# Kernel tuning notes

Measured on AMD Instinct MI355X. Metric: run time of the kernel, lower is better.

The kernel has to match this reference:

```python
import jax, jax.numpy as jnp
import numpy as np

N, D, H = 50000, 256, 8
C = D // H  # 32
E = 1600000
NEG_SLOPE = 0.2  # GATConv default leaky_relu slope
EPS = 1e-5


def setup_inputs() -> dict:
    key = jax.random.key(0)
    ks = jax.random.split(key, 8)
    x = jax.random.normal(ks[0], (N, D), dtype=jnp.float32)
    edge_index = jax.random.randint(ks[1], (2, E), 0, N, dtype=jnp.int32)
    # GATConv params: lin (no bias), att_src/att_dst, output bias
    scale = 1.0 / np.sqrt(D)
    W = jax.random.normal(ks[2], (D, H * C), dtype=jnp.float32) * scale
    att_src = jax.random.normal(ks[3], (H, C), dtype=jnp.float32) * scale
    att_dst = jax.random.normal(ks[4], (H, C), dtype=jnp.float32) * scale
    bias = jnp.zeros((H * C,), dtype=jnp.float32)
    ln_w = jnp.ones((D,), dtype=jnp.float32)
    ln_b = jnp.zeros((D,), dtype=jnp.float32)
    return {"x": x, "edge_index": edge_index, "W": W, "att_src": att_src,
            "att_dst": att_dst, "bias": bias, "ln_w": ln_w, "ln_b": ln_b}


def _gat_block(x, src, dst, W, att_src, att_dst, bias, ln_w, ln_b):
    n = x.shape[0]
    h = (x @ W).reshape(n, H, C)                      # [N,H,C]
    a_src = jnp.einsum('nhc,hc->nh', h, att_src)      # [N,H]
    a_dst = jnp.einsum('nhc,hc->nh', h, att_dst)      # [N,H]
    e = a_src[src] + a_dst[dst]                       # [E',H]
    e = jnp.where(e > 0, e, NEG_SLOPE * e)            # leaky_relu
    # segment softmax over incoming edges of each dst node
    m = jax.ops.segment_max(e, dst, num_segments=n)   # [N,H]
    m = jnp.where(jnp.isfinite(m), m, 0.0)
    ex = jnp.exp(e - m[dst])
    denom = jax.ops.segment_sum(ex, dst, num_segments=n)  # [N,H]
    alpha = ex / denom[dst]                           # [E',H] (self-loops => denom>0)
    msg = h[src] * alpha[..., None]                   # [E',H,C]
    out = jax.ops.segment_sum(msg, dst, num_segments=n).reshape(n, H * C) + bias
    # residual + LayerNorm
    y = out + x
    mu = y.mean(axis=-1, keepdims=True)
    var = y.var(axis=-1, keepdims=True)
    return (y - mu) / jnp.sqrt(var + EPS) * ln_w + ln_b


def reference(x, edge_index, W, att_src, att_dst, bias, ln_w, ln_b):
    n = x.shape[0]
    loop = jnp.arange(n, dtype=edge_index.dtype)      # GATConv adds self-loops by default
    src = jnp.concatenate([edge_index[0], loop])
    dst = jnp.concatenate([edge_index[1], loop])
    return _gat_block(x, src, dst, W, att_src, att_dst, bias, ln_w, ln_b)
```

## Files before the change

kernel.cpp:

```cpp
#include <hip/hip_runtime.h>

#define D_ 256
#define H_ 8
#define C_ 32
#define CAP_ 128
#define NEG_SLOPE 0.2f
#define EPS_ 1e-5f

typedef __attribute__((ext_vector_type(8))) short bf16x8;
typedef __attribute__((ext_vector_type(4))) float f32x4;
typedef __attribute__((ext_vector_type(2))) float f32x2;

__device__ __forceinline__ unsigned pk2(float a, float b) {
  unsigned ua = __float_as_uint(a), ub = __float_as_uint(b);
  ua = (ua + 0x7fffu + ((ua >> 16) & 1u)) >> 16;
  ub = (ub + 0x7fffu + ((ub >> 16) & 1u)) >> 16;
  return ua | (ub << 16);
}
__device__ __forceinline__ unsigned short f2b(float a) {
  unsigned ua = __float_as_uint(a);
  return (unsigned short)((ua + 0x7fffu + ((ua >> 16) & 1u)) >> 16);
}

#if defined(__has_builtin)
#if __has_builtin(__builtin_amdgcn_cvt_pk_fp8_f32) && __has_builtin(__builtin_amdgcn_cvt_pk_f32_fp8)
#define HW_FP8 1
#endif
#endif

__device__ __forceinline__ unsigned enc2_fp8(float a, float b) {
#ifdef HW_FP8
  return ((unsigned)__builtin_amdgcn_cvt_pk_fp8_f32(a, b, 0, false)) & 0xffffu;
#else
  unsigned r = 0;
  float vv[2] = {a, b};
  #pragma unroll
  for (int i = 0; i < 2; i++) {
    float v = vv[i];
    unsigned u = __float_as_uint(v);
    unsigned s = (u >> 31) << 7;
    float av = fabsf(v);
    unsigned byte;
    if (av < 0.015625f) byte = s;
    else if (av >= 448.f) byte = s | 0x7e;
    else {
      unsigned ua = u & 0x7fffffffu;
      ua += 0x0007ffffu + ((ua >> 20) & 1u);
      unsigned e = (ua >> 23) - 120u;
      unsigned m = (ua >> 20) & 7u;
      byte = s | (e << 3) | m;
    }
    r |= byte << (8 * i);
  }
  return r;
#endif
}

__device__ __forceinline__ float dec1_fp8(unsigned b) {
  unsigned s = (b >> 7) & 1u, em = b & 0x7fu;
  float v = (em >= 8u) ? __uint_as_float((((em >> 3) + 120u) << 23) | ((em & 7u) << 20))
                       : (float)em * 0.001953125f;
  return s ? -v : v;
}

__device__ __forceinline__ void dec4_fp8(unsigned q, float& f0, float& f1, float& f2, float& f3) {
#ifdef HW_FP8
  f32x2 lo = __builtin_amdgcn_cvt_pk_f32_fp8((int)q, false);
  f32x2 hi = __builtin_amdgcn_cvt_pk_f32_fp8((int)q, true);
  f0 = lo[0]; f1 = lo[1]; f2 = hi[0]; f3 = hi[1];
#else
  f0 = dec1_fp8(q & 0xffu); f1 = dec1_fp8((q >> 8) & 0xffu);
  f2 = dec1_fp8((q >> 16) & 0xffu); f3 = dec1_fp8(q >> 24);
#endif
}

__global__ __launch_bounds__(256) void k_prep_zero(const float* __restrict__ W,
    unsigned short* __restrict__ Wt, int* __restrict__ cnt, int N) {
  if (blockIdx.x < 256) {
    int i = blockIdx.x * 256 + threadIdx.x;
    int n = i >> 8, k = i & 255;
    Wt[i] = f2b(W[k * 256 + n]);
  } else {
    int n = (blockIdx.x - 256) * 256 + threadIdx.x;
    if (n < N) cnt[n] = 0;
  }
}

__global__ __launch_bounds__(256) void k_hist_gemm(const float* __restrict__ x,
    const unsigned short* __restrict__ Wt, unsigned char* __restrict__ h,
    const int* __restrict__ ei, int* __restrict__ cnt, int* __restrict__ bucket,
    const float* __restrict__ att_src, const float* __restrict__ att_dst,
    float* __restrict__ asrc, float* __restrict__ adst,
    int E, int N, int GB, int TOT) {
  const long long bid = blockIdx.x;
  const long long gid = (bid * GB) / TOT;
  const bool isg = ((bid + 1) * GB) / TOT > gid;
  if (!isg) {
    int hb = (int)(bid - gid);
    int e = hb * 256 + threadIdx.x;
    if (e < E) {
      int s = ei[e], d = ei[E + e];
      int r = atomicAdd(&cnt[d], 1);
      if (r < CAP_) bucket[(size_t)d * CAP_ + r] = s;
    }
    return;
  }
  __shared__ uint4 As4[64 * 4];
  __shared__ uint4 Bs4[256 * 4];
  const int tid = threadIdx.x;
  const int bm = (int)gid * 64;
  const int w = tid >> 6, l = tid & 63;
  const int lrow = l & 15, lk = l >> 4;
  f32x4 acc[4][4];
  #pragma unroll
  for (int m = 0; m < 4; m++)
    #pragma unroll
    for (int n = 0; n < 4; n++) acc[m][n] = (f32x4){0.f, 0.f, 0.f, 0.f};

  const int ar = tid >> 2, aq = tid & 3;
  const bool arv = (bm + ar) < N;
  const float* axp = x + (size_t)(bm + ar) * 256 + aq * 8;
  const unsigned short* bwp = Wt + (size_t)tid * 256;
  const int bx = (tid >> 1) & 3;

  const int hh0 = 2 * w, hh1 = 2 * w + 1;
  const float as00 = att_src[hh0 * 32 + lrow], as01 = att_src[hh0 * 32 + 16 + lrow];
  const float as10 = att_src[hh1 * 32 + lrow], as11 = att_src[hh1 * 32 + 16 + lrow];
  const float ad00 = att_dst[hh0 * 32 + lrow], ad01 = att_dst[hh0 * 32 + 16 + lrow];
  const float ad10 = att_dst[hh1 * 32 + lrow], ad11 = att_dst[hh1 * 32 + 16 + lrow];

  for (int k0 = 0; k0 < 256; k0 += 32) {
    float4 v0 = make_float4(0.f, 0.f, 0.f, 0.f), v1 = v0;
    if (arv) {
      v0 = *(const float4*)(axp + k0);
      v1 = *(const float4*)(axp + k0 + 4);
    }
    uint4 ap;
    ap.x = pk2(v0.x, v0.y); ap.y = pk2(v0.z, v0.w);
    ap.z = pk2(v1.x, v1.y); ap.w = pk2(v1.z, v1.w);
    uint4 b0 = *(const uint4*)(bwp + k0);
    uint4 b1 = *(const uint4*)(bwp + k0 + 8);
    uint4 b2 = *(const uint4*)(bwp + k0 + 16);
    uint4 b3 = *(const uint4*)(bwp + k0 + 24);
    __syncthreads();
    As4[ar * 4 + (aq ^ ((ar >> 1) & 3))] = ap;
    Bs4[tid * 4 + (0 ^ bx)] = b0;
    Bs4[tid * 4 + (1 ^ bx)] = b1;
    Bs4[tid * 4 + (2 ^ bx)] = b2;
    Bs4[tid * 4 + (3 ^ bx)] = b3;
    __syncthreads();
    bf16x8 a[4], b[4];
    #pragma unroll
    for (int m = 0; m < 4; m++) {
      int r = m * 16 + lrow;
      a[m] = *(const bf16x8*)&As4[r * 4 + (lk ^ ((r >> 1) & 3))];
    }
    #pragma unroll
    for (int n = 0; n < 4; n++) {
      int rb = w * 64 + n * 16 + lrow;
      b[n] = *(const bf16x8*)&Bs4[rb * 4 + (lk ^ ((rb >> 1) & 3))];
    }
    #pragma unroll
    for (int m = 0; m < 4; m++)
      #pragma unroll
      for (int n = 0; n < 4; n++)
        acc[m][n] = __builtin_amdgcn_mfma_f32_16x16x32_bf16(a[m], b[n], acc[m][n], 0, 0, 0);
  }
  #pragma unroll
  for (int m = 0; m < 4; m++) {
    #pragma unroll
    for (int reg = 0; reg < 4; reg++) {
      int row = bm + m * 16 + lk * 4 + reg;
      float v0 = acc[m][0][reg], v1 = acc[m][1][reg];
      float v2 = acc[m][2][reg], v3 = acc[m][3][reg];
      if (row < N) {
        unsigned pa = enc2_fp8(v0, v1);
        unsigned pb = enc2_fp8(v2, v3);
        unsigned char* hp = h + (size_t)row * 256 + w * 64 + lrow;
        hp[0]  = (unsigned char)(pa & 0xff);
        hp[16] = (unsigned char)((pa >> 8) & 0xff);
        hp[32] = (unsigned char)(pb & 0xff);
        hp[48] = (unsigned char)((pb >> 8) & 0xff);
      }
      float ps0 = v0 * as00 + v1 * as01;
      float ps1 = v2 * as10 + v3 * as11;
      float pd0 = v0 * ad00 + v1 * ad01;
      float pd1 = v2 * ad10 + v3 * ad11;
      #pragma unroll
      for (int off = 1; off < 16; off <<= 1) {
        ps0 += __shfl_xor(ps0, off);
        ps1 += __shfl_xor(ps1, off);
        pd0 += __shfl_xor(pd0, off);
        pd1 += __shfl_xor(pd1, off);
      }
      if (lrow == 0 && row < N) {
        asrc[row * 8 + hh0] = ps0;
        asrc[row * 8 + hh1] = ps1;
        adst[row * 8 + hh0] = pd0;
        adst[row * 8 + hh1] = pd1;
      }
    }
  }
}

__global__ __launch_bounds__(256) void k_gather(const int* __restrict__ cnt,
    const int* __restrict__ bucket, const float* __restrict__ asrc,
    const float* __restrict__ adst, const unsigned char* __restrict__ h,
    const float* __restrict__ x, const float* __restrict__ bias,
    const float* __restrict__ lnw, const float* __restrict__ lnb,
    float* __restrict__ out, int N) {
  int wid = (blockIdx.x * 256 + threadIdx.x) >> 6;
  if (wid >= N) return;
  const int lane = threadIdx.x & 63;
  const int hd = lane >> 3;
  const char* __restrict__ hB = (const char*)h;
  const char* __restrict__ aB = (const char*)asrc;
  const unsigned hoff = (unsigned)lane * 4u;
  const unsigned aoff = (unsigned)hd * 4u;
  const float ad = adst[((unsigned)wid << 3) + hd];

  float a_self = *(const float*)(aB + (((unsigned)wid) << 5) + aoff) + ad;
  a_self = a_self > 0.f ? a_self : NEG_SLOPE * a_self;
  float m = a_self, ssum = 1.f;
  float acc0, acc1, acc2, acc3;
  {
    unsigned qs = *(const unsigned*)(hB + (((unsigned)wid) << 8) + hoff);
    dec4_fp8(qs, acc0, acc1, acc2, acc3);
  }

  const int len = min(cnt[wid], CAP_);
  const int* __restrict__ bp = bucket + (size_t)wid * CAP_;
  int i = 0;
  for (; i + 8 <= len; i += 8) {
    int4 sA = *(const int4*)(bp + i);
    int4 sB = *(const int4*)(bp + i + 4);
    float a0 = *(const float*)(aB + (((unsigned)sA.x) << 5) + aoff) + ad;
    float a1 = *(const float*)(aB + (((unsigned)sA.y) << 5) + aoff) + ad;
    float a2 = *(const float*)(aB + (((unsigned)sA.z) << 5) + aoff) + ad;
    float a3 = *(const float*)(aB + (((unsigned)sA.w) << 5) + aoff) + ad;
    float a4 = *(const float*)(aB + (((unsigned)sB.x) << 5) + aoff) + ad;
    float a5 = *(const float*)(aB + (((unsigned)sB.y) << 5) + aoff) + ad;
    float a6 = *(const float*)(aB + (((unsigned)sB.z) << 5) + aoff) + ad;
    float a7 = *(const float*)(aB + (((unsigned)sB.w) << 5) + aoff) + ad;
    unsigned q0 = *(const unsigned*)(hB + (((unsigned)sA.x) << 8) + hoff);
    unsigned q1 = *(const unsigned*)(hB + (((unsigned)sA.y) << 8) + hoff);
    unsigned q2 = *(const unsigned*)(hB + (((unsigned)sA.z) << 8) + hoff);
    unsigned q3 = *(const unsigned*)(hB + (((unsigned)sA.w) << 8) + hoff);
    unsigned q4 = *(const unsigned*)(hB + (((unsigned)sB.x) << 8) + hoff);
    unsigned q5 = *(const unsigned*)(hB + (((unsigned)sB.y) << 8) + hoff);
    unsigned q6 = *(const unsigned*)(hB + (((unsigned)sB.z) << 8) + hoff);
    unsigned q7 = *(const unsigned*)(hB + (((unsigned)sB.w) << 8) + hoff);
    a0 = a0 > 0.f ? a0 : NEG_SLOPE * a0;
    a1 = a1 > 0.f ? a1 : NEG_SLOPE * a1;
    a2 = a2 > 0.f ? a2 : NEG_SLOPE * a2;
    a3 = a3 > 0.f ? a3 : NEG_SLOPE * a3;
    a4 = a4 > 0.f ? a4 : NEG_SLOPE * a4;
    a5 = a5 > 0.f ? a5 : NEG_SLOPE * a5;
    a6 = a6 > 0.f ? a6 : NEG_SLOPE * a6;
    a7 = a7 > 0.f ? a7 : NEG_SLOPE * a7;
    float mx = fmaxf(fmaxf(fmaxf(a0, a1), fmaxf(a2, a3)),
                     fmaxf(fmaxf(a4, a5), fmaxf(a6, a7)));
    if (mx - m > 8.f) {
      float r = __expf(m - mx);
      acc0 *= r; acc1 *= r; acc2 *= r; acc3 *= r; ssum *= r; m = mx;
    }
    float p0 = __expf(a0 - m), p1 = __expf(a1 - m);
    float p2 = __expf(a2 - m), p3 = __expf(a3 - m);
    float p4 = __expf(a4 - m), p5 = __expf(a5 - m);
    float p6 = __expf(a6 - m), p7 = __expf(a7 - m);
    ssum += ((p0 + p1) + (p2 + p3)) + ((p4 + p5) + (p6 + p7));
    float f0, f1, f2, f3;
    dec4_fp8(q0, f0, f1, f2, f3);
    acc0 = fmaf(p0, f0, acc0); acc1 = fmaf(p0, f1, acc1);
    acc2 = fmaf(p0, f2, acc2); acc3 = fmaf(p0, f3, acc3);
    dec4_fp8(q1, f0, f1, f2, f3);
    acc0 = fmaf(p1, f0, acc0); acc1 = fmaf(p1, f1, acc1);
    acc2 = fmaf(p1, f2, acc2); acc3 = fmaf(p1, f3, acc3);
    dec4_fp8(q2, f0, f1, f2, f3);
    acc0 = fmaf(p2, f0, acc0); acc1 = fmaf(p2, f1, acc1);
    acc2 = fmaf(p2, f2, acc2); acc3 = fmaf(p2, f3, acc3);
    dec4_fp8(q3, f0, f1, f2, f3);
    acc0 = fmaf(p3, f0, acc0); acc1 = fmaf(p3, f1, acc1);
    acc2 = fmaf(p3, f2, acc2); acc3 = fmaf(p3, f3, acc3);
    dec4_fp8(q4, f0, f1, f2, f3);
    acc0 = fmaf(p4, f0, acc0); acc1 = fmaf(p4, f1, acc1);
    acc2 = fmaf(p4, f2, acc2); acc3 = fmaf(p4, f3, acc3);
    dec4_fp8(q5, f0, f1, f2, f3);
    acc0 = fmaf(p5, f0, acc0); acc1 = fmaf(p5, f1, acc1);
    acc2 = fmaf(p5, f2, acc2); acc3 = fmaf(p5, f3, acc3);
    dec4_fp8(q6, f0, f1, f2, f3);
    acc0 = fmaf(p6, f0, acc0); acc1 = fmaf(p6, f1, acc1);
    acc2 = fmaf(p6, f2, acc2); acc3 = fmaf(p6, f3, acc3);
    dec4_fp8(q7, f0, f1, f2, f3);
    acc0 = fmaf(p7, f0, acc0); acc1 = fmaf(p7, f1, acc1);
    acc2 = fmaf(p7, f2, acc2); acc3 = fmaf(p7, f3, acc3);
  }
  for (; i < len; ++i) {
    int s0 = bp[i];
    float a0 = *(const float*)(aB + (((unsigned)s0) << 5) + aoff) + ad;
    unsigned q0 = *(const unsigned*)(hB + (((unsigned)s0) << 8) + hoff);
    a0 = a0 > 0.f ? a0 : NEG_SLOPE * a0;
    if (a0 - m > 8.f) {
      float r = __expf(m - a0);
      acc0 *= r; acc1 *= r; acc2 *= r; acc3 *= r; ssum *= r; m = a0;
    }
    float p0 = __expf(a0 - m);
    ssum += p0;
    float f0, f1, f2, f3;
    dec4_fp8(q0, f0, f1, f2, f3);
    acc0 = fmaf(p0, f0, acc0); acc1 = fmaf(p0, f1, acc1);
    acc2 = fmaf(p0, f2, acc2); acc3 = fmaf(p0, f3, acc3);
  }
  const float inv = 1.f / ssum;

  const int c0 = lane * 4;
  float4 xb = *(const float4*)(x + (size_t)wid * D_ + c0);
  float4 bb = *(const float4*)(bias + c0);
  float y0 = acc0 * inv + bb.x + xb.x;
  float y1 = acc1 * inv + bb.y + xb.y;
  float y2 = acc2 * inv + bb.z + xb.z;
  float y3 = acc3 * inv + bb.w + xb.w;
  float sv = y0 + y1 + y2 + y3;
  float qv = y0 * y0 + y1 * y1 + y2 * y2 + y3 * y3;
  #pragma unroll
  for (int off = 1; off < 64; off <<= 1) {
    sv += __shfl_xor(sv, off);
    qv += __shfl_xor(qv, off);
  }
  float mu = sv * (1.f / 256.f);
  float var = qv * (1.f / 256.f) - mu * mu;
  float rs = rsqrtf(var + EPS_);
  float4 lw = *(const float4*)(lnw + c0);
  float4 lb = *(const float4*)(lnb + c0);
  float4 o;
  o.x = (y0 - mu) * rs * lw.x + lb.x;
  o.y = (y1 - mu) * rs * lw.y + lb.y;
  o.z = (y2 - mu) * rs * lw.z + lb.z;
  o.w = (y3 - mu) * rs * lw.w + lb.w;
  *(float4*)(out + (size_t)wid * D_ + c0) = o;
}

extern "C" void kernel_launch(void* const* d_in, const int* in_sizes, int n_in,
                              void* d_out, int out_size, void* d_ws, size_t ws_size,
                              hipStream_t stream) {
  const float* x       = (const float*)d_in[0];
  const int*   ei      = (const int*)d_in[1];
  const float* W       = (const float*)d_in[2];
  const float* att_src = (const float*)d_in[3];
  const float* att_dst = (const float*)d_in[4];
  const float* bias    = (const float*)d_in[5];
  const float* lnw     = (const float*)d_in[6];
  const float* lnb     = (const float*)d_in[7];
  const int N = in_sizes[0] / D_;
  const int E = in_sizes[1] / 2;
  float* out = (float*)d_out;

  char* w = (char*)d_ws;
  unsigned short* Wt = (unsigned short*)w; w += (size_t)256 * 256 * 2;
  unsigned char*  h  = (unsigned char*)w;  w += (size_t)N * D_;
  w += ((size_t)16 - ((size_t)w & 15)) & 15;
  float* asrc   = (float*)w; w += (size_t)N * H_ * 4;
  float* adst   = (float*)w; w += (size_t)N * H_ * 4;
  int*   cnt    = (int*)w;   w += (size_t)N * 4;
  int*   bucket = (int*)w;   w += (size_t)N * CAP_ * 4;

  k_prep_zero<<<256 + (N + 255) / 256, 256, 0, stream>>>(W, Wt, cnt, N);

  const int HB = (E + 255) / 256;
  const int GB = (N + 63) / 64;
  const int TOT = HB + GB;
  k_hist_gemm<<<TOT, 256, 0, stream>>>(x, Wt, h, ei, cnt, bucket,
                                       att_src, att_dst, asrc, adst, E, N, GB, TOT);

  k_gather<<<(N * 64 + 255) / 256, 256, 0, stream>>>(cnt, bucket, asrc, adst, h,
                                                     x, bias, lnw, lnb, out, N);
}
```

Measured before the change: 182.7 us.

## Enlarge GEMM tile to 128 rows with 512-thread blocks and memset counters

The fused histogram+GEMM kernel moves to 512-thread blocks. The GEMM tile doubles to 128 rows with 8 waves in a 2x4 grid, so each staged Wt tile is reused across twice as many rows. Histogram blocks now cover 512 edges each. Counter zeroing moves from the prep kernel to hipMemsetAsync, which adds an extra stream operation but shrinks the prep launch. Larger blocks may lower occupancy and increase register pressure.

```diff
diff --git a/kernel.cpp b/kernel.cpp
--- a/kernel.cpp
+++ b/kernel.cpp
@@ -74,19 +74,14 @@
 #endif
 }
 
-__global__ __launch_bounds__(256) void k_prep_zero(const float* __restrict__ W,
-    unsigned short* __restrict__ Wt, int* __restrict__ cnt, int N) {
-  if (blockIdx.x < 256) {
-    int i = blockIdx.x * 256 + threadIdx.x;
-    int n = i >> 8, k = i & 255;
-    Wt[i] = f2b(W[k * 256 + n]);
-  } else {
-    int n = (blockIdx.x - 256) * 256 + threadIdx.x;
-    if (n < N) cnt[n] = 0;
-  }
-}
-
-__global__ __launch_bounds__(256) void k_hist_gemm(const float* __restrict__ x,
+__global__ __launch_bounds__(256) void k_prep(const float* __restrict__ W,
+    unsigned short* __restrict__ Wt) {
+  int i = blockIdx.x * 256 + threadIdx.x;
+  int n = i >> 8, k = i & 255;
+  Wt[i] = f2b(W[k * 256 + n]);
+}
+
+__global__ __launch_bounds__(512) void k_hist_gemm(const float* __restrict__ x,
     const unsigned short* __restrict__ Wt, unsigned char* __restrict__ h,
     const int* __restrict__ ei, int* __restrict__ cnt, int* __restrict__ bucket,
     const float* __restrict__ att_src, const float* __restrict__ att_dst,
@@ -95,9 +90,10 @@
   const long long bid = blockIdx.x;
   const long long gid = (bid * GB) / TOT;
   const bool isg = ((bid + 1) * GB) / TOT > gid;
+  const int tid = threadIdx.x;
   if (!isg) {
     int hb = (int)(bid - gid);
-    int e = hb * 256 + threadIdx.x;
+    int e = hb * 512 + tid;
     if (e < E) {
       int s = ei[e], d = ei[E + e];
       int r = atomicAdd(&cnt[d], 1);
@@ -105,11 +101,11 @@
     }
     return;
   }
-  __shared__ uint4 As4[64 * 4];
+  __shared__ uint4 As4[128 * 4];
   __shared__ uint4 Bs4[256 * 4];
-  const int tid = threadIdx.x;
-  const int bm = (int)gid * 64;
+  const int bm = (int)gid * 128;
   const int w = tid >> 6, l = tid & 63;
+  const int wr = w >> 2, wc = w & 3;
   const int lrow = l & 15, lk = l >> 4;
   f32x4 acc[4][4];
   #pragma unroll
@@ -120,14 +116,9 @@
   const int ar = tid >> 2, aq = tid & 3;
   const bool arv = (bm + ar) < N;
   const float* axp = x + (size_t)(bm + ar) * 256 + aq * 8;
-  const unsigned short* bwp = Wt + (size_t)tid * 256;
-  const int bx = (tid >> 1) & 3;
-
-  const int hh0 = 2 * w, hh1 = 2 * w + 1;
-  const float as00 = att_src[hh0 * 32 + lrow], as01 = att_src[hh0 * 32 + 16 + lrow];
-  const float as10 = att_src[hh1 * 32 + lrow], as11 = att_src[hh1 * 32 + 16 + lrow];
-  const float ad00 = att_dst[hh0 * 32 + lrow], ad01 = att_dst[hh0 * 32 + 16 + lrow];
-  const float ad10 = att_dst[hh1 * 32 + lrow], ad11 = att_dst[hh1 * 32 + 16 + lrow];
+  const int br = tid >> 1, bh = tid & 1;
+  const unsigned short* bwp = Wt + (size_t)br * 256 + bh * 16;
+  const int bxs = (br >> 1) & 3;
 
   for (int k0 = 0; k0 < 256; k0 += 32) {
     float4 v0 = make_float4(0.f, 0.f, 0.f, 0.f), v1 = v0;
@@ -140,24 +131,20 @@
     ap.z = pk2(v1.x, v1.y); ap.w = pk2(v1.z, v1.w);
     uint4 b0 = *(const uint4*)(bwp + k0);
     uint4 b1 = *(const uint4*)(bwp + k0 + 8);
-    uint4 b2 = *(const uint4*)(bwp + k0 + 16);
-    uint4 b3 = *(const uint4*)(bwp + k0 + 24);
     __syncthreads();
     As4[ar * 4 + (aq ^ ((ar >> 1) & 3))] = ap;
-    Bs4[tid * 4 + (0 ^ bx)] = b0;
-    Bs4[tid * 4 + (1 ^ bx)] = b1;
-    Bs4[tid * 4 + (2 ^ bx)] = b2;
-    Bs4[tid * 4 + (3 ^ bx)] = b3;
+    Bs4[br * 4 + ((2 * bh + 0) ^ bxs)] = b0;
+    Bs4[br * 4 + ((2 * bh + 1) ^ bxs)] = b1;
     __syncthreads();
     bf16x8 a[4], b[4];
     #pragma unroll
     for (int m = 0; m < 4; m++) {
-      int r = m * 16 + lrow;
+      int r = wr * 64 + m * 16 + lrow;
       a[m] = *(const bf16x8*)&As4[r * 4 + (lk ^ ((r >> 1) & 3))];
     }
     #pragma unroll
     for (int n = 0; n < 4; n++) {
-      int rb = w * 64 + n * 16 + lrow;
+      int rb = wc * 64 + n * 16 + lrow;
       b[n] = *(const bf16x8*)&Bs4[rb * 4 + (lk ^ ((rb >> 1) & 3))];
     }
     #pragma unroll
@@ -166,17 +153,22 @@
       for (int n = 0; n < 4; n++)
         acc[m][n] = __builtin_amdgcn_mfma_f32_16x16x32_bf16(a[m], b[n], acc[m][n], 0, 0, 0);
   }
+  const int hh0 = 2 * wc, hh1 = 2 * wc + 1;
+  const float as00 = att_src[hh0 * 32 + lrow], as01 = att_src[hh0 * 32 + 16 + lrow];
+  const float as10 = att_src[hh1 * 32 + lrow], as11 = att_src[hh1 * 32 + 16 + lrow];
+  const float ad00 = att_dst[hh0 * 32 + lrow], ad01 = att_dst[hh0 * 32 + 16 + lrow];
+  const float ad10 = att_dst[hh1 * 32 + lrow], ad11 = att_dst[hh1 * 32 + 16 + lrow];
   #pragma unroll
   for (int m = 0; m < 4; m++) {
     #pragma unroll
     for (int reg = 0; reg < 4; reg++) {
-      int row = bm + m * 16 + lk * 4 + reg;
+      int row = bm + wr * 64 + m * 16 + lk * 4 + reg;
       float v0 = acc[m][0][reg], v1 = acc[m][1][reg];
       float v2 = acc[m][2][reg], v3 = acc[m][3][reg];
       if (row < N) {
         unsigned pa = enc2_fp8(v0, v1);
         unsigned pb = enc2_fp8(v2, v3);
-        unsigned char* hp = h + (size_t)row * 256 + w * 64 + lrow;
+        unsigned char* hp = h + (size_t)row * 256 + wc * 64 + lrow;
         hp[0]  = (unsigned char)(pa & 0xff);
         hp[16] = (unsigned char)((pa >> 8) & 0xff);
         hp[32] = (unsigned char)(pb & 0xff);
@@ -364,12 +356,13 @@
   int*   cnt    = (int*)w;   w += (size_t)N * 4;
   int*   bucket = (int*)w;   w += (size_t)N * CAP_ * 4;
 
-  k_prep_zero<<<256 + (N + 255) / 256, 256, 0, stream>>>(W, Wt, cnt, N);
-
-  const int HB = (E + 255) / 256;
-  const int GB = (N + 63) / 64;
+  hipMemsetAsync(cnt, 0, (size_t)N * 4, stream);
+  k_prep<<<256, 256, 0, stream>>>(W, Wt);
+
+  const int HB = (E + 511) / 512;
+  const int GB = (N + 127) / 128;
   const int TOT = HB + GB;
-  k_hist_gemm<<<TOT, 256, 0, stream>>>(x, Wt, h, ei, cnt, bucket,
+  k_hist_gemm<<<TOT, 512, 0, stream>>>(x, Wt, h, ei, cnt, bucket,
                                        att_src, att_dst, asrc, adst, E, N, GB, TOT);
 
   k_gather<<<(N * 64 + 255) / 256, 256, 0, stream>>>(cnt, bucket, asrc, adst, h,
```

After: 184.0 us. No clear change (+0.7%).
